# Performance work log

Hardware: AMD Instinct MI355X
Metric: run time of the kernel (lower is better)

## Reference

```python
import jax, jax.numpy as jnp
import numpy as np

N = 262144
L = 16; FEAT = 2; T = 1 << 19; N_MIN = 16; N_MAX = 4096
AABB = 1.0
TIME_RES1 = 16; TIME_RES2 = 20
B = float(np.exp(np.log(N_MAX / N_MIN) / (L - 1)))
SCALES = [N_MIN * (B ** l) - 1.0 for l in range(L)]
RES = [int(np.ceil(s)) + 1 for s in SCALES]
PRIMES = (np.uint32(1), np.uint32(2654435761), np.uint32(805459861))
OFFS = np.array([[(i >> d) & 1 for d in range(3)] for i in range(8)], dtype=np.int32)  # [8,3]


def hash_encode(x, table):
    """Instant-NGP multiresolution hash encoding. x: [N,3] in [0,1], table: [L,T,F] -> [N,L*F]."""
    offs = jnp.asarray(OFFS)
    outs = []
    for l in range(L):
        s = SCALES[l]; res = RES[l]
        pos = x * s + 0.5
        p0 = jnp.floor(pos)
        w = pos - p0                                             # [N,3] trilinear weights
        c = p0.astype(jnp.int32)[:, None, :] + offs[None, :, :]  # [N,8,3] corner coords
        if res ** 3 <= T:
            # dense grid fits in table -> coherent indexing (tcnn behavior)
            idx = c[..., 0] + c[..., 1] * res + c[..., 2] * (res * res)
        else:
            cu = c.astype(jnp.uint32)
            idx = ((cu[..., 0] * PRIMES[0]) ^ (cu[..., 1] * PRIMES[1]) ^ (cu[..., 2] * PRIMES[2])) & np.uint32(T - 1)
            idx = idx.astype(jnp.int32)
        wv = jnp.prod(jnp.where(offs[None] == 1, w[:, None, :], 1.0 - w[:, None, :]), axis=-1)  # [N,8]
        outs.append(jnp.einsum('nkf,nk->nf', table[l][idx], wv))
    return jnp.concatenate(outs, axis=1)


def sh_encode(dirs):
    """tcnn SphericalHarmonics degree 4: dirs in [0,1] mapped to [-1,1] -> 16 coeffs."""
    d = dirs * 2.0 - 1.0
    x, y, z = d[:, 0], d[:, 1], d[:, 2]
    xy, xz, yz = x * y, x * z, y * z
    x2, y2, z2 = x * x, y * y, z * z
    cols = [
        jnp.full_like(x, 0.28209479177387814),
        -0.48860251190291987 * y,
        0.48860251190291987 * z,
        -0.48860251190291987 * x,
        1.0925484305920792 * xy,
        -1.0925484305920792 * yz,
        0.94617469575755997 * z2 - 0.31539156525252005,
        -1.0925484305920792 * xz,
        0.54627421529603959 * (x2 - y2),
        0.59004358992664352 * y * (-3.0 * x2 + y2),
        2.8906114426405538 * xy * z,
        0.45704579946446572 * y * (1.0 - 5.0 * z2),
        0.3731763325901154 * z * (5.0 * z2 - 3.0),
        0.45704579946446572 * x * (1.0 - 5.0 * z2),
        1.4453057213202769 * z * (x2 - y2),
        0.59004358992664352 * x * (-x2 + 3.0 * y2),
    ]
    return jnp.stack(cols, axis=1)


def setup_inputs() -> dict:
    key = jax.random.key(0)
    ks = jax.random.split(key, 12)
    xyz = jax.random.uniform(ks[0], (N, 3), minval=-AABB, maxval=AABB, dtype=jnp.float32)
    tcol = jnp.full((N, 1), 0.37, dtype=jnp.float32)  # one shared time per chunk (module reads ts[0])
    original_xyzs = jnp.concatenate([xyz, tcol], axis=1)
    dirs = jax.random.uniform(ks[1], (N, 3), dtype=jnp.float32)
    tinit = lambda k: jax.random.normal(k, (L, T, FEAT), dtype=jnp.float32) * 1e-2
    lin = lambda k, fi, fo: jax.random.normal(k, (fi, fo), dtype=jnp.float32) * (1.0 / np.sqrt(fi))
    return dict(
        original_xyzs=original_xyzs, dirs=dirs,
        table_a1=tinit(ks[2]), table_a2=tinit(ks[3]),       # xyz_hashes[index], xyz_hashes[index+1]
        table_b1=tinit(ks[4]), table_b2=tinit(ks[5]),       # xyz_hashes2[index2], xyz_hashes2[index2+1]
        table_static=tinit(ks[6]),
        w_xyz1=lin(ks[7], 96, 64), w_xyz2=lin(ks[8], 64, 16),
        w_c1=lin(ks[9], 32, 64), w_c2=lin(ks[10], 64, 64), w_c3=lin(ks[11], 64, 3),
    )


def reference(original_xyzs, dirs, table_a1, table_a2, table_b1, table_b2, table_static,
              w_xyz1, w_xyz2, w_c1, w_c2, w_c3):
    t = original_xyzs[0, 3]
    xyz = (original_xyzs[:, :3] + AABB) / AABB / 2.0        # [-aabb,aabb] -> [0,1]
    prev1 = 1.0 - (t * TIME_RES1 - jnp.floor(t * TIME_RES1)); next1 = 1.0 - prev1
    s1 = prev1 + next1; prev1 = prev1 / s1; next1 = next1 / s1
    prev2 = 1.0 - (t * TIME_RES2 - jnp.floor(t * TIME_RES2)); next2 = 1.0 - prev2
    s2 = prev2 + next2; prev2 = prev2 / s2; next2 = next2 / s2
    fa1 = hash_encode(xyz, table_a1); fa2 = hash_encode(xyz, table_a2)
    fb1 = hash_encode(xyz, table_b1); fb2 = hash_encode(xyz, table_b2)
    blend_a = fa1 * prev1 + fa2 * next1
    blend_b = fb1 * prev2 + fb2 * next2
    hash_res = jnp.concatenate([blend_a, blend_b, hash_encode(xyz, table_static)], axis=1)  # [N,96]
    h = jax.nn.relu(hash_res @ w_xyz1) @ w_xyz2              # [N,16]
    sigma = jnp.exp(h[:, 0])                                 # TruncExp forward
    dir_enc = sh_encode(dirs)                                # [N,16]
    ch = jnp.concatenate([dir_enc, h], axis=1)               # [N,32]
    color = jax.nn.sigmoid(jax.nn.relu(jax.nn.relu(ch @ w_c1) @ w_c2) @ w_c3)
    feature1 = jnp.concatenate([fa1[:, -8:], fb1[:, -8:]], axis=1)
    feature2 = jnp.concatenate([fa2[:, -8:], fb2[:, -8:]], axis=1)
    return color, sigma, feature1, feature2
```

## Files before the change

### kernel.cpp

```cpp
#include <hip/hip_runtime.h>
#include <cmath>

constexpr int NPTS = 262144;
constexpr int LVLS = 16;
constexpr int TSZ  = 524288;
constexpr unsigned TMASK = TSZ - 1u;
constexpr unsigned P1 = 2654435761u;
constexpr unsigned P2 = 805459861u;

constexpr size_t PB10_BYTES = (size_t)LVLS * TSZ * 8;
constexpr size_t AB4_BYTES  = (size_t)4 * TSZ * 16;
constexpr size_t FEAT_BYTES = (size_t)LVLS * 3 * NPTS * 4;
constexpr int    WP_W1 = 0,    WP_W1N = 48 * 64;
constexpr int    WP_W2 = 3072, WP_W2N = 32 * 16;
constexpr int    WP_C1 = 3584, WP_C1N = 16 * 64;
constexpr int    WP_C2 = 4608, WP_C2N = 32 * 64;
constexpr int    WP_TOT = 6656;
constexpr size_t WP_BYTES = WP_TOT * 4;
constexpr size_t WS_NEED = PB10_BYTES + AB4_BYTES + FEAT_BYTES + WP_BYTES;

constexpr float QSCALE = 4096.0f;
constexpr float QINV   = 1.0f / 4096.0f;

typedef __fp16 half2v __attribute__((ext_vector_type(2)));

__device__ __forceinline__ half2v pkh(float lo, float hi) {
  return __builtin_amdgcn_cvt_pkrtz(lo, hi);
}
__device__ __forceinline__ unsigned pkh2(float lo, float hi) {
  half2v r = __builtin_amdgcn_cvt_pkrtz(lo, hi);
  return *reinterpret_cast<unsigned*>(&r);
}
__device__ __forceinline__ half2v ash2(unsigned w) {
  return *reinterpret_cast<half2v*>(&w);
}
__device__ __forceinline__ float2 uph2(unsigned w) {
  half2v h = ash2(w);
  return make_float2((float)h.x, (float)h.y);
}

#if __has_builtin(__builtin_amdgcn_fdot2)
__device__ __forceinline__ float DOT2(half2v a, half2v b, float c) {
  return __builtin_amdgcn_fdot2(a, b, c, false);
}
#else
__device__ __forceinline__ float DOT2(half2v a, half2v b, float c) {
  return c + (float)a.x * (float)b.x + (float)a.y * (float)b.y;
}
#endif

__device__ __forceinline__ void time_weights(float t, float mul, float& bp, float& bn) {
  const float ft = t * mul;
  const float fr = ft - floorf(ft);
  float p = 1.0f - fr, n = 1.0f - p;
  const float s = p + n;
  bp = p / s; bn = n / s;
}

__device__ __forceinline__ unsigned q10(float v) {
  int q = (int)floorf(v * QSCALE + 0.5f) + 512;
  q = (q < 0) ? 0 : ((q > 1023) ? 1023 : q);
  return (unsigned)q;
}
__device__ __forceinline__ float dq10(unsigned w, int sh) {
  return (float)((int)((w >> sh) & 1023u) - 512);
}

constexpr int MAXS = 10;
struct Sched {
  float scale[LVLS];
  int   res[LVLS];
  int   dense[LVLS];
  int   nblocks[8];
  int   nsegs[8];
  int   sblk0[8][MAXS];
  unsigned char skind[8][MAXS];
  unsigned char slevel[8][MAXS];
  short schunk0[8][MAXS];
};

__global__ __launch_bounds__(256)
void repack_pb(const float* __restrict__ xyzs,
               const float2* __restrict__ ta1, const float2* __restrict__ ta2,
               const float2* __restrict__ tb1, const float2* __restrict__ tb2,
               const float2* __restrict__ tst,
               uint2* __restrict__ PB10, uint4* __restrict__ AB4)
{
  const size_t i = (size_t)blockIdx.x * 256 + threadIdx.x;
  const int l = (int)(i >> 19);
  float p1w, n1w, p2w, n2w;
  const float t = xyzs[3];
  time_weights(t, 16.0f, p1w, n1w);
  time_weights(t, 20.0f, p2w, n2w);
  const float2 a1 = ta1[i], a2 = ta2[i], b1 = tb1[i], b2 = tb2[i], st = tst[i];
  const float ba0 = a1.x * p1w + a2.x * n1w;
  const float ba1v = a1.y * p1w + a2.y * n1w;
  const float bb0 = b1.x * p2w + b2.x * n2w;
  const float bb1v = b1.y * p2w + b2.y * n2w;
  uint2 e;
  e.x = q10(ba0) | (q10(ba1v) << 10) | (q10(bb0) << 20);
  e.y = q10(bb1v) | (q10(st.x) << 10) | (q10(st.y) << 20);
  PB10[i] = e;
  if (l >= 12) {
    uint4 r;
    r.x = pkh2(a1.x, a1.y);
    r.y = pkh2(a2.x, a2.y);
    r.z = pkh2(b1.x, b1.y);
    r.w = pkh2(b2.x, b2.y);
    AB4[i - (size_t)12 * TSZ] = r;
  }
}

__global__ __launch_bounds__(256)
void wconv(const float* __restrict__ w1, const float* __restrict__ w2,
           const float* __restrict__ wc1, const float* __restrict__ wc2,
           unsigned* __restrict__ wp)
{
  const int g = blockIdx.x * 256 + threadIdx.x;
  if (g < WP_W1N) {
    const int i = g, r = i >> 6, j = i & 63;
    wp[WP_W1 + i] = pkh2(w1[(2 * r) * 64 + j], w1[(2 * r + 1) * 64 + j]);
  } else if (g < WP_W1N + WP_W2N) {
    const int i = g - WP_W1N, r = i >> 4, j = i & 15;
    wp[WP_W2 + i] = pkh2(w2[(2 * r) * 16 + j], w2[(2 * r + 1) * 16 + j]);
  } else if (g < WP_W1N + WP_W2N + WP_C1N) {
    const int i = g - WP_W1N - WP_W2N, r = i >> 6, j = i & 63;
    wp[WP_C1 + i] = pkh2(wc1[(2 * r) * 64 + j], wc1[(2 * r + 1) * 64 + j]);
  } else if (g < WP_TOT) {
    const int i = g - WP_W1N - WP_W2N - WP_C1N, r = i >> 6, j = i & 63;
    wp[WP_C2 + i] = pkh2(wc2[(2 * r) * 64 + j], wc2[(2 * r + 1) * 64 + j]);
  }
}

__global__ __launch_bounds__(512)
void ngp_gather(const float* __restrict__ xyzs,
                const uint2* __restrict__ PB10, const uint4* __restrict__ AB4,
                unsigned* __restrict__ feat, float* __restrict__ out, Sched sc)
{
  const int k = blockIdx.x & 7;
  const int j = blockIdx.x >> 3;
  if (j >= sc.nblocks[k]) return;
  int l = 0, chunk = 0, kind = 0;
  #pragma unroll
  for (int s = 0; s < MAXS; ++s) {
    if (s < sc.nsegs[k] && j >= sc.sblk0[k][s]) {
      kind  = sc.skind[k][s];
      l     = sc.slevel[k][s];
      chunk = sc.schunk0[k][s] + (j - sc.sblk0[k][s]);
    }
  }
  const int p = (chunk << 9) + threadIdx.x;

  const float4 xin = reinterpret_cast<const float4*>(xyzs)[p];
  const float px = (xin.x + 1.0f) * 0.5f;
  const float py = (xin.y + 1.0f) * 0.5f;
  const float pz = (xin.z + 1.0f) * 0.5f;

  const float s = sc.scale[l];
  const int res = sc.res[l];
  const float fx = px * s + 0.5f; const float f0x = floorf(fx); const float wx = fx - f0x;
  const float fy = py * s + 0.5f; const float f0y = floorf(fy); const float wy = fy - f0y;
  const float fz = pz * s + 0.5f; const float f0z = floorf(fz); const float wz = fz - f0z;
  const int ix = (int)f0x, iy = (int)f0y, iz = (int)f0z;

  unsigned idx[8];
  if (sc.dense[l]) {
    const int r2 = res * res;
    const int bx0 = ix,       bx1 = ix + 1;
    const int by0 = iy * res, by1 = by0 + res;
    const int bz0 = iz * r2,  bz1 = bz0 + r2;
    idx[0] = (unsigned)(bx0 + by0 + bz0);
    idx[1] = (unsigned)(bx1 + by0 + bz0);
    idx[2] = (unsigned)(bx0 + by1 + bz0);
    idx[3] = (unsigned)(bx1 + by1 + bz0);
    idx[4] = (unsigned)(bx0 + by0 + bz1);
    idx[5] = (unsigned)(bx1 + by0 + bz1);
    idx[6] = (unsigned)(bx0 + by1 + bz1);
    idx[7] = (unsigned)(bx1 + by1 + bz1);
  } else {
    const unsigned hx0 = (unsigned)ix,      hx1 = hx0 + 1u;
    const unsigned hy0 = (unsigned)iy * P1, hy1 = hy0 + P1;
    const unsigned hz0 = (unsigned)iz * P2, hz1 = hz0 + P2;
    idx[0] = (hx0 ^ hy0 ^ hz0) & TMASK;
    idx[1] = (hx1 ^ hy0 ^ hz0) & TMASK;
    idx[2] = (hx0 ^ hy1 ^ hz0) & TMASK;
    idx[3] = (hx1 ^ hy1 ^ hz0) & TMASK;
    idx[4] = (hx0 ^ hy0 ^ hz1) & TMASK;
    idx[5] = (hx1 ^ hy0 ^ hz1) & TMASK;
    idx[6] = (hx0 ^ hy1 ^ hz1) & TMASK;
    idx[7] = (hx1 ^ hy1 ^ hz1) & TMASK;
  }

  const float wxa = 1.0f - wx, wya = 1.0f - wy, wza = 1.0f - wz;
  float wv[8];
  wv[0] = wxa * wya * wza;
  wv[1] = wx  * wya * wza;
  wv[2] = wxa * wy  * wza;
  wv[3] = wx  * wy  * wza;
  wv[4] = wxa * wya * wz;
  wv[5] = wx  * wya * wz;
  wv[6] = wxa * wy  * wz;
  wv[7] = wx  * wy  * wz;

  if (kind == 0) {
    const uint2* tb = PB10 + (size_t)l * TSZ;
    uint2 m[8];
    #pragma unroll
    for (int c = 0; c < 8; ++c) m[c] = tb[idx[c]];
    float A0 = 0.f, A1 = 0.f, B0 = 0.f, B1 = 0.f, S0 = 0.f, S1 = 0.f;
    #pragma unroll
    for (int c = 0; c < 8; ++c) {
      const float w = wv[c];
      const unsigned ux = m[c].x, uy = m[c].y;
      A0 += dq10(ux, 0)  * w;
      A1 += dq10(ux, 10) * w;
      B0 += dq10(ux, 20) * w;
      B1 += dq10(uy, 0)  * w;
      S0 += dq10(uy, 10) * w;
      S1 += dq10(uy, 20) * w;
    }
    feat[(size_t)(l * 3 + 0) * NPTS + p] = pkh2(A0 * QINV, A1 * QINV);
    feat[(size_t)(l * 3 + 1) * NPTS + p] = pkh2(B0 * QINV, B1 * QINV);
    feat[(size_t)(l * 3 + 2) * NPTS + p] = pkh2(S0 * QINV, S1 * QINV);
  } else {
    const uint4* tb = AB4 + (size_t)(l - 12) * TSZ;
    uint4 m[8];
    #pragma unroll
    for (int c = 0; c < 8; ++c) m[c] = tb[idx[c]];
    float a10 = 0.f, a11 = 0.f, a20 = 0.f, a21 = 0.f;
    float b10 = 0.f, b11 = 0.f, b20 = 0.f, b21 = 0.f;
    #pragma unroll
    for (int c = 0; c < 8; ++c) {
      const float w = wv[c];
      float2 f;
      f = uph2(m[c].x); a10 += f.x * w; a11 += f.y * w;
      f = uph2(m[c].y); a20 += f.x * w; a21 += f.y * w;
      f = uph2(m[c].z); b10 += f.x * w; b11 += f.y * w;
      f = uph2(m[c].w); b20 += f.x * w; b21 += f.y * w;
    }
    const size_t fo = (size_t)(l - 12) * 2;
    const size_t f1base = (size_t)4 * NPTS + (size_t)p * 16;
    const size_t f2base = (size_t)20 * NPTS + (size_t)p * 16;
    *reinterpret_cast<float2*>(out + f1base + fo)     = make_float2(a10, a11);
    *reinterpret_cast<float2*>(out + f1base + 8 + fo) = make_float2(b10, b11);
    *reinterpret_cast<float2*>(out + f2base + fo)     = make_float2(a20, a21);
    *reinterpret_cast<float2*>(out + f2base + 8 + fo) = make_float2(b20, b21);
  }
}

__global__ __launch_bounds__(256)
void ngp_mlp(const float* __restrict__ dirs,
             const unsigned* __restrict__ feat,
             const unsigned* __restrict__ wp,
             const float* __restrict__ wc3,
             float* __restrict__ out)
{
  __shared__ unsigned sw[WP_TOT];
  __shared__ float swc3[192];
  for (int i = threadIdx.x; i < WP_TOT; i += 256) sw[i] = wp[i];
  for (int i = threadIdx.x; i < 192; i += 256) swc3[i] = wc3[i];
  __syncthreads();

  const int n = blockIdx.x * 256 + threadIdx.x;
  const half2v* w1p = reinterpret_cast<const half2v*>(sw + WP_W1);
  const half2v* w2p = reinterpret_cast<const half2v*>(sw + WP_W2);
  const half2v* c1p = reinterpret_cast<const half2v*>(sw + WP_C1);
  const half2v* c2p = reinterpret_cast<const half2v*>(sw + WP_C2);

  float h1[64];
  #pragma unroll
  for (int j = 0; j < 64; ++j) h1[j] = 0.0f;

  for (int l = 0; l < LVLS; ++l) {
    const half2v A2 = ash2(feat[(size_t)(l * 3 + 0) * NPTS + n]);
    const half2v B2 = ash2(feat[(size_t)(l * 3 + 1) * NPTS + n]);
    const half2v S2 = ash2(feat[(size_t)(l * 3 + 2) * NPTS + n]);
    #pragma unroll
    for (int j = 0; j < 64; ++j) {
      float acc = h1[j];
      acc = DOT2(A2, w1p[l * 64 + j], acc);
      acc = DOT2(B2, w1p[(16 + l) * 64 + j], acc);
      acc = DOT2(S2, w1p[(32 + l) * 64 + j], acc);
      h1[j] = acc;
    }
  }

  float h2[16];
  #pragma unroll
  for (int j = 0; j < 16; ++j) h2[j] = 0.0f;
  #pragma unroll
  for (int k = 0; k < 32; ++k) {
    const half2v hp = pkh(fmaxf(h1[2 * k], 0.0f), fmaxf(h1[2 * k + 1], 0.0f));
    #pragma unroll
    for (int j = 0; j < 16; ++j) h2[j] = DOT2(hp, w2p[k * 16 + j], h2[j]);
  }

  out[(size_t)3 * NPTS + n] = expf(h2[0]);

  const float dx = dirs[(size_t)n * 3 + 0] * 2.0f - 1.0f;
  const float dy = dirs[(size_t)n * 3 + 1] * 2.0f - 1.0f;
  const float dz = dirs[(size_t)n * 3 + 2] * 2.0f - 1.0f;
  const float xy = dx * dy, xz = dx * dz, yz = dy * dz;
  const float x2 = dx * dx, y2 = dy * dy, z2 = dz * dz;
  float sh[16];
  sh[0]  = 0.28209479177387814f;
  sh[1]  = -0.48860251190291987f * dy;
  sh[2]  = 0.48860251190291987f * dz;
  sh[3]  = -0.48860251190291987f * dx;
  sh[4]  = 1.0925484305920792f * xy;
  sh[5]  = -1.0925484305920792f * yz;
  sh[6]  = 0.94617469575756f * z2 - 0.31539156525252005f;
  sh[7]  = -1.0925484305920792f * xz;
  sh[8]  = 0.5462742152960396f * (x2 - y2);
  sh[9]  = 0.5900435899266435f * dy * (-3.0f * x2 + y2);
  sh[10] = 2.890611442640554f * xy * dz;
  sh[11] = 0.4570457994644657f * dy * (1.0f - 5.0f * z2);
  sh[12] = 0.3731763325901154f * dz * (5.0f * z2 - 3.0f);
  sh[13] = 0.4570457994644657f * dx * (1.0f - 5.0f * z2);
  sh[14] = 1.445305721320277f * dz * (x2 - y2);
  sh[15] = 0.5900435899266435f * dx * (-x2 + 3.0f * y2);

  half2v chp[16];
  #pragma unroll
  for (int r = 0; r < 8; ++r) chp[r] = pkh(sh[2 * r], sh[2 * r + 1]);
  #pragma unroll
  for (int r = 0; r < 8; ++r) chp[8 + r] = pkh(h2[2 * r], h2[2 * r + 1]);
  float r1[64];
  #pragma unroll
  for (int j = 0; j < 64; ++j) r1[j] = 0.0f;
  #pragma unroll
  for (int k = 0; k < 16; ++k) {
    const half2v cp = chp[k];
    #pragma unroll
    for (int j = 0; j < 64; ++j) r1[j] = DOT2(cp, c1p[k * 64 + j], r1[j]);
  }

  float r2[64];
  #pragma unroll
  for (int j = 0; j < 64; ++j) r2[j] = 0.0f;
  #pragma unroll
  for (int k = 0; k < 32; ++k) {
    const half2v rp = pkh(fmaxf(r1[2 * k], 0.0f), fmaxf(r1[2 * k + 1], 0.0f));
    #pragma unroll
    for (int j = 0; j < 64; ++j) r2[j] = DOT2(rp, c2p[k * 64 + j], r2[j]);
  }

  float c0a = 0.f, c1a = 0.f, c2a = 0.f;
  #pragma unroll
  for (int k = 0; k < 64; ++k) {
    const float a = fmaxf(r2[k], 0.0f);
    c0a += a * swc3[k * 3 + 0];
    c1a += a * swc3[k * 3 + 1];
    c2a += a * swc3[k * 3 + 2];
  }
  out[(size_t)n * 3 + 0] = 1.0f / (1.0f + expf(-c0a));
  out[(size_t)n * 3 + 1] = 1.0f / (1.0f + expf(-c1a));
  out[(size_t)n * 3 + 2] = 1.0f / (1.0f + expf(-c2a));
}

__global__ __launch_bounds__(256)
void ngp_fused(const float* __restrict__ xyzs, const float* __restrict__ dirs,
               const float* __restrict__ ta1, const float* __restrict__ ta2,
               const float* __restrict__ tb1, const float* __restrict__ tb2,
               const float* __restrict__ tst,
               const float* __restrict__ w1, const float* __restrict__ w2,
               const float* __restrict__ wc1, const float* __restrict__ wc2,
               const float* __restrict__ wc3, float* __restrict__ out, Sched sc)
{
  const int n = blockIdx.x * 256 + threadIdx.x;
  if (n >= NPTS) return;

  float prev1, next1, prev2, next2;
  const float t = xyzs[3];
  time_weights(t, 16.0f, prev1, next1);
  time_weights(t, 20.0f, prev2, next2);

  const float4 xin = reinterpret_cast<const float4*>(xyzs)[n];
  const float px = (xin.x + 1.0f) * 0.5f;
  const float py = (xin.y + 1.0f) * 0.5f;
  const float pz = (xin.z + 1.0f) * 0.5f;

  float h1[64];
  #pragma unroll
  for (int j = 0; j < 64; ++j) h1[j] = 0.0f;

  const size_t f1base = (size_t)4 * NPTS + (size_t)n * 16;
  const size_t f2base = (size_t)20 * NPTS + (size_t)n * 16;

  for (int l = 0; l < LVLS; ++l) {
    const float s = sc.scale[l];
    const int res = sc.res[l];
    const float fx = px * s + 0.5f; const float f0x = floorf(fx); const float wx = fx - f0x;
    const float fy = py * s + 0.5f; const float f0y = floorf(fy); const float wy = fy - f0y;
    const float fz = pz * s + 0.5f; const float f0z = floorf(fz); const float wz = fz - f0z;
    const int ix = (int)f0x, iy = (int)f0y, iz = (int)f0z;

    unsigned idx[8];
    if (sc.dense[l]) {
      const int r2 = res * res;
      const int bx0 = ix,       bx1 = ix + 1;
      const int by0 = iy * res, by1 = by0 + res;
      const int bz0 = iz * r2,  bz1 = bz0 + r2;
      idx[0] = (unsigned)(bx0 + by0 + bz0);
      idx[1] = (unsigned)(bx1 + by0 + bz0);
      idx[2] = (unsigned)(bx0 + by1 + bz0);
      idx[3] = (unsigned)(bx1 + by1 + bz0);
      idx[4] = (unsigned)(bx0 + by0 + bz1);
      idx[5] = (unsigned)(bx1 + by0 + bz1);
      idx[6] = (unsigned)(bx0 + by1 + bz1);
      idx[7] = (unsigned)(bx1 + by1 + bz1);
    } else {
      const unsigned hx0 = (unsigned)ix,      hx1 = hx0 + 1u;
      const unsigned hy0 = (unsigned)iy * P1, hy1 = hy0 + P1;
      const unsigned hz0 = (unsigned)iz * P2, hz1 = hz0 + P2;
      idx[0] = (hx0 ^ hy0 ^ hz0) & TMASK;
      idx[1] = (hx1 ^ hy0 ^ hz0) & TMASK;
      idx[2] = (hx0 ^ hy1 ^ hz0) & TMASK;
      idx[3] = (hx1 ^ hy1 ^ hz0) & TMASK;
      idx[4] = (hx0 ^ hy0 ^ hz1) & TMASK;
      idx[5] = (hx1 ^ hy0 ^ hz1) & TMASK;
      idx[6] = (hx0 ^ hy1 ^ hz1) & TMASK;
      idx[7] = (hx1 ^ hy1 ^ hz1) & TMASK;
    }

    const float wxa = 1.0f - wx, wya = 1.0f - wy, wza = 1.0f - wz;
    float wv[8];
    wv[0] = wxa * wya * wza;
    wv[1] = wx  * wya * wza;
    wv[2] = wxa * wy  * wza;
    wv[3] = wx  * wy  * wza;
    wv[4] = wxa * wya * wz;
    wv[5] = wx  * wya * wz;
    wv[6] = wxa * wy  * wz;
    wv[7] = wx  * wy  * wz;

    float a10 = 0.f, a11 = 0.f, a20 = 0.f, a21 = 0.f;
    float b10 = 0.f, b11 = 0.f, b20 = 0.f, b21 = 0.f;
    float st0 = 0.f, st1 = 0.f;
    const size_t lbase = (size_t)l * TSZ;

    const float2* ba1 = reinterpret_cast<const float2*>(ta1) + lbase;
    const float2* ba2 = reinterpret_cast<const float2*>(ta2) + lbase;
    const float2* bb1 = reinterpret_cast<const float2*>(tb1) + lbase;
    const float2* bb2 = reinterpret_cast<const float2*>(tb2) + lbase;
    const float2* bst = reinterpret_cast<const float2*>(tst) + lbase;
    float2 va1[8], va2[8], vb1[8], vb2[8], vst[8];
    #pragma unroll
    for (int c = 0; c < 8; ++c) {
      const unsigned id = idx[c];
      va1[c] = ba1[id]; va2[c] = ba2[id]; vb1[c] = bb1[id];
      vb2[c] = bb2[id]; vst[c] = bst[id];
    }
    #pragma unroll
    for (int c = 0; c < 8; ++c) {
      const float w = wv[c];
      a10 += va1[c].x * w; a11 += va1[c].y * w;
      a20 += va2[c].x * w; a21 += va2[c].y * w;
      b10 += vb1[c].x * w; b11 += vb1[c].y * w;
      b20 += vb2[c].x * w; b21 += vb2[c].y * w;
      st0 += vst[c].x * w; st1 += vst[c].y * w;
    }

    const float ba0f = a10 * prev1 + a20 * next1;
    const float ba1f = a11 * prev1 + a21 * next1;
    const float bb0f = b10 * prev2 + b20 * next2;
    const float bb1f = b11 * prev2 + b21 * next2;

    const float* wr0 = w1 + (size_t)(2 * l) * 64;
    const float* wr1 = w1 + (size_t)(2 * l + 1) * 64;
    const float* wr2 = w1 + (size_t)(32 + 2 * l) * 64;
    const float* wr3 = w1 + (size_t)(33 + 2 * l) * 64;
    const float* wr4 = w1 + (size_t)(64 + 2 * l) * 64;
    const float* wr5 = w1 + (size_t)(65 + 2 * l) * 64;
    #pragma unroll
    for (int j = 0; j < 64; ++j) {
      float acc = h1[j];
      acc += ba0f * wr0[j];
      acc += ba1f * wr1[j];
      acc += bb0f * wr2[j];
      acc += bb1f * wr3[j];
      acc += st0  * wr4[j];
      acc += st1  * wr5[j];
      h1[j] = acc;
    }

    if (l >= 12) {
      const size_t fo = (size_t)(l - 12) * 2;
      float2* o;
      o = reinterpret_cast<float2*>(out + f1base + fo);     *o = make_float2(a10, a11);
      o = reinterpret_cast<float2*>(out + f1base + 8 + fo); *o = make_float2(b10, b11);
      o = reinterpret_cast<float2*>(out + f2base + fo);     *o = make_float2(a20, a21);
      o = reinterpret_cast<float2*>(out + f2base + 8 + fo); *o = make_float2(b20, b21);
    }
  }

  float h2[16];
  #pragma unroll
  for (int j = 0; j < 16; ++j) h2[j] = 0.0f;
  #pragma unroll
  for (int k = 0; k < 64; ++k) {
    const float a = fmaxf(h1[k], 0.0f);
    #pragma unroll
    for (int j = 0; j < 16; ++j) h2[j] += a * w2[k * 16 + j];
  }
  out[(size_t)3 * NPTS + n] = expf(h2[0]);

  const float dx = dirs[(size_t)n * 3 + 0] * 2.0f - 1.0f;
  const float dy = dirs[(size_t)n * 3 + 1] * 2.0f - 1.0f;
  const float dz = dirs[(size_t)n * 3 + 2] * 2.0f - 1.0f;
  const float xy = dx * dy, xz = dx * dz, yz = dy * dz;
  const float x2 = dx * dx, y2 = dy * dy, z2 = dz * dz;
  float sh[16];
  sh[0]  = 0.28209479177387814f;
  sh[1]  = -0.48860251190291987f * dy;
  sh[2]  = 0.48860251190291987f * dz;
  sh[3]  = -0.48860251190291987f * dx;
  sh[4]  = 1.0925484305920792f * xy;
  sh[5]  = -1.0925484305920792f * yz;
  sh[6]  = 0.94617469575756f * z2 - 0.31539156525252005f;
  sh[7]  = -1.0925484305920792f * xz;
  sh[8]  = 0.5462742152960396f * (x2 - y2);
  sh[9]  = 0.5900435899266435f * dy * (-3.0f * x2 + y2);
  sh[10] = 2.890611442640554f * xy * dz;
  sh[11] = 0.4570457994644657f * dy * (1.0f - 5.0f * z2);
  sh[12] = 0.3731763325901154f * dz * (5.0f * z2 - 3.0f);
  sh[13] = 0.4570457994644657f * dx * (1.0f - 5.0f * z2);
  sh[14] = 1.445305721320277f * dz * (x2 - y2);
  sh[15] = 0.5900435899266435f * dx * (-x2 + 3.0f * y2);

  float r1[64];
  #pragma unroll
  for (int j = 0; j < 64; ++j) r1[j] = 0.0f;
  #pragma unroll
  for (int k = 0; k < 16; ++k) {
    const float a = sh[k];
    #pragma unroll
    for (int j = 0; j < 64; ++j) r1[j] += a * wc1[(size_t)k * 64 + j];
  }
  #pragma unroll
  for (int k = 0; k < 16; ++k) {
    const float a = h2[k];
    #pragma unroll
    for (int j = 0; j < 64; ++j) r1[j] += a * wc1[(size_t)(16 + k) * 64 + j];
  }
  #pragma unroll
  for (int j = 0; j < 64; ++j) r1[j] = fmaxf(r1[j], 0.0f);

  float r2[64];
  #pragma unroll
  for (int j = 0; j < 64; ++j) r2[j] = 0.0f;
  #pragma unroll
  for (int k = 0; k < 64; ++k) {
    const float a = r1[k];
    #pragma unroll
    for (int j = 0; j < 64; ++j) r2[j] += a * wc2[(size_t)k * 64 + j];
  }

  float c0a = 0.f, c1a = 0.f, c2a = 0.f;
  #pragma unroll
  for (int k = 0; k < 64; ++k) {
    const float a = fmaxf(r2[k], 0.0f);
    c0a += a * wc3[k * 3 + 0];
    c1a += a * wc3[k * 3 + 1];
    c2a += a * wc3[k * 3 + 2];
  }
  out[(size_t)n * 3 + 0] = 1.0f / (1.0f + expf(-c0a));
  out[(size_t)n * 3 + 1] = 1.0f / (1.0f + expf(-c1a));
  out[(size_t)n * 3 + 2] = 1.0f / (1.0f + expf(-c2a));
}

extern "C" void kernel_launch(void* const* d_in, const int* in_sizes, int n_in,
                              void* d_out, int out_size, void* d_ws, size_t ws_size,
                              hipStream_t stream) {
  const float* xyzs = (const float*)d_in[0];
  const float* dirs = (const float*)d_in[1];
  const float* ta1  = (const float*)d_in[2];
  const float* ta2  = (const float*)d_in[3];
  const float* tb1  = (const float*)d_in[4];
  const float* tb2  = (const float*)d_in[5];
  const float* tst  = (const float*)d_in[6];
  const float* w1   = (const float*)d_in[7];
  const float* w2   = (const float*)d_in[8];
  const float* wc1  = (const float*)d_in[9];
  const float* wc2  = (const float*)d_in[10];
  const float* wc3  = (const float*)d_in[11];

  Sched sc = {};
  const double B = exp(log(4096.0 / 16.0) / 15.0);
  for (int l = 0; l < LVLS; ++l) {
    const double s = 16.0 * pow(B, (double)l) - 1.0;
    sc.scale[l] = (float)s;
    const int res = (int)ceil(s) + 1;
    sc.res[l] = res;
    sc.dense[l] = ((long long)res * res * res <= (long long)TSZ) ? 1 : 0;
  }

  struct Unit { int kind, level; long long w; };
  Unit units[20];
  int nu = 0;
  for (int l = 0; l < LVLS; ++l) units[nu++] = {0, l, sc.dense[l] ? 1LL : 2LL};
  for (int l = 12; l < LVLS; ++l) units[nu++] = {1, l, 3LL};

  constexpr int CH = 512;
  {
    long long totW = 0;
    for (int u = 0; u < nu; ++u) totW += units[u].w * CH;
    int k = 0;
    long long acc = 0;
    auto target = [&](int kk) { return (totW * (kk + 1)) / 8; };
    for (int u = 0; u < nu; ++u) {
      int c0 = 0;
      const long long w = units[u].w;
      while (c0 < CH) {
        while (k < 7 && (acc >= target(k) || sc.nsegs[k] >= MAXS)) k++;
        long long room = target(k) - acc;
        int take;
        if (k == 7) take = CH - c0;
        else {
          take = (int)((room + w - 1) / w);
          if (take > CH - c0) take = CH - c0;
          if (take <= 0) take = 1;
        }
        const int sgi = sc.nsegs[k];
        sc.skind[k][sgi]   = (unsigned char)units[u].kind;
        sc.slevel[k][sgi]  = (unsigned char)units[u].level;
        sc.schunk0[k][sgi] = (short)c0;
        sc.sblk0[k][sgi]   = sc.nblocks[k];
        sc.nsegs[k]++;
        sc.nblocks[k] += take;
        acc += (long long)take * w;
        c0 += take;
      }
    }
  }
  int maxblk = 0;
  for (int k = 0; k < 8; ++k) if (sc.nblocks[k] > maxblk) maxblk = sc.nblocks[k];

  if (ws_size >= WS_NEED) {
    char* base = (char*)d_ws;
    uint2*    PB10 = (uint2*)base;
    uint4*    AB4  = (uint4*)(base + PB10_BYTES);
    unsigned* feat = (unsigned*)(base + PB10_BYTES + AB4_BYTES);
    unsigned* wpp  = (unsigned*)(base + PB10_BYTES + AB4_BYTES + FEAT_BYTES);

    repack_pb<<<(LVLS * TSZ) / 256, 256, 0, stream>>>(
        xyzs, (const float2*)ta1, (const float2*)ta2, (const float2*)tb1,
        (const float2*)tb2, (const float2*)tst, PB10, AB4);
    wconv<<<(WP_TOT + 255) / 256, 256, 0, stream>>>(w1, w2, wc1, wc2, wpp);
    ngp_gather<<<8 * maxblk, 512, 0, stream>>>(
        xyzs, PB10, AB4, feat, (float*)d_out, sc);
    ngp_mlp<<<NPTS / 256, 256, 0, stream>>>(dirs, feat, wpp, wc3, (float*)d_out);
  } else {
    ngp_fused<<<NPTS / 256, 256, 0, stream>>>(
        xyzs, dirs, ta1, ta2, tb1, tb2, tst,
        w1, w2, wc1, wc2, wc3, (float*)d_out, sc);
  }
}
```

Baseline: 360.6 us.

## Merge top-level gathers into single 12-bit packed table pass

For levels 12-15, the separate PB10 (blended 10-bit) and AB4 (fp16 a1/a2/b1/b2) tables are replaced by one 16-byte entry holding all ten channels quantized to 12 bits. That entry includes the static features. The gather kernel now does one 8-corner gather per point for those levels instead of two, and it computes the time blend itself while writing both the MLP features and the per-timestep outputs. This removes four level-gather units and the PB10 writes for those levels. In exchange it adds 64-bit unpacking work and reduces precision from fp16 to 12-bit fixed point for the feature outputs.

```diff
diff --git a/kernel.cpp b/kernel.cpp
--- a/kernel.cpp
+++ b/kernel.cpp
@@ -7,9 +7,10 @@
 constexpr unsigned TMASK = TSZ - 1u;
 constexpr unsigned P1 = 2654435761u;
 constexpr unsigned P2 = 805459861u;
-
-constexpr size_t PB10_BYTES = (size_t)LVLS * TSZ * 8;
-constexpr size_t AB4_BYTES  = (size_t)4 * TSZ * 16;
+constexpr int NPB = 12;
+
+constexpr size_t PB10_BYTES = (size_t)NPB * TSZ * 8;
+constexpr size_t ABQ_BYTES  = (size_t)4 * TSZ * 16;
 constexpr size_t FEAT_BYTES = (size_t)LVLS * 3 * NPTS * 4;
 constexpr int    WP_W1 = 0,    WP_W1N = 48 * 64;
 constexpr int    WP_W2 = 3072, WP_W2N = 32 * 16;
@@ -17,10 +18,12 @@
 constexpr int    WP_C2 = 4608, WP_C2N = 32 * 64;
 constexpr int    WP_TOT = 6656;
 constexpr size_t WP_BYTES = WP_TOT * 4;
-constexpr size_t WS_NEED = PB10_BYTES + AB4_BYTES + FEAT_BYTES + WP_BYTES;
+constexpr size_t WS_NEED = PB10_BYTES + ABQ_BYTES + FEAT_BYTES + WP_BYTES;
 
 constexpr float QSCALE = 4096.0f;
 constexpr float QINV   = 1.0f / 4096.0f;
+constexpr float QS12   = 16384.0f;
+constexpr float QI12   = 1.0f / 16384.0f;
 
 typedef __fp16 half2v __attribute__((ext_vector_type(2)));
 
@@ -33,10 +36,6 @@
 }
 __device__ __forceinline__ half2v ash2(unsigned w) {
   return *reinterpret_cast<half2v*>(&w);
-}
-__device__ __forceinline__ float2 uph2(unsigned w) {
-  half2v h = ash2(w);
-  return make_float2((float)h.x, (float)h.y);
 }
 
 #if __has_builtin(__builtin_amdgcn_fdot2)
@@ -64,6 +63,14 @@
 }
 __device__ __forceinline__ float dq10(unsigned w, int sh) {
   return (float)((int)((w >> sh) & 1023u) - 512);
+}
+__device__ __forceinline__ unsigned long long q12(float v) {
+  int q = (int)floorf(v * QS12 + 0.5f) + 2048;
+  q = (q < 0) ? 0 : ((q > 4095) ? 4095 : q);
+  return (unsigned long long)q;
+}
+__device__ __forceinline__ float dq12(unsigned long long u, int sh) {
+  return (float)((int)((u >> sh) & 4095ull) - 2048);
 }
 
 constexpr int MAXS = 10;
@@ -84,30 +91,35 @@
                const float2* __restrict__ ta1, const float2* __restrict__ ta2,
                const float2* __restrict__ tb1, const float2* __restrict__ tb2,
                const float2* __restrict__ tst,
-               uint2* __restrict__ PB10, uint4* __restrict__ AB4)
+               uint2* __restrict__ PB10, uint4* __restrict__ ABQ)
 {
   const size_t i = (size_t)blockIdx.x * 256 + threadIdx.x;
   const int l = (int)(i >> 19);
-  float p1w, n1w, p2w, n2w;
-  const float t = xyzs[3];
-  time_weights(t, 16.0f, p1w, n1w);
-  time_weights(t, 20.0f, p2w, n2w);
   const float2 a1 = ta1[i], a2 = ta2[i], b1 = tb1[i], b2 = tb2[i], st = tst[i];
-  const float ba0 = a1.x * p1w + a2.x * n1w;
-  const float ba1v = a1.y * p1w + a2.y * n1w;
-  const float bb0 = b1.x * p2w + b2.x * n2w;
-  const float bb1v = b1.y * p2w + b2.y * n2w;
-  uint2 e;
-  e.x = q10(ba0) | (q10(ba1v) << 10) | (q10(bb0) << 20);
-  e.y = q10(bb1v) | (q10(st.x) << 10) | (q10(st.y) << 20);
-  PB10[i] = e;
-  if (l >= 12) {
-    uint4 r;
-    r.x = pkh2(a1.x, a1.y);
-    r.y = pkh2(a2.x, a2.y);
-    r.z = pkh2(b1.x, b1.y);
-    r.w = pkh2(b2.x, b2.y);
-    AB4[i - (size_t)12 * TSZ] = r;
+  if (l < NPB) {
+    float p1w, n1w, p2w, n2w;
+    const float t = xyzs[3];
+    time_weights(t, 16.0f, p1w, n1w);
+    time_weights(t, 20.0f, p2w, n2w);
+    const float ba0  = a1.x * p1w + a2.x * n1w;
+    const float ba1v = a1.y * p1w + a2.y * n1w;
+    const float bb0  = b1.x * p2w + b2.x * n2w;
+    const float bb1v = b1.y * p2w + b2.y * n2w;
+    uint2 e;
+    e.x = q10(ba0) | (q10(ba1v) << 10) | (q10(bb0) << 20);
+    e.y = q10(bb1v) | (q10(st.x) << 10) | (q10(st.y) << 20);
+    PB10[i] = e;
+  } else {
+    const unsigned long long lo =
+        q12(a1.x) | (q12(a1.y) << 12) | (q12(a2.x) << 24) |
+        (q12(a2.y) << 36) | (q12(st.x) << 48);
+    const unsigned long long hi =
+        q12(b1.x) | (q12(b1.y) << 12) | (q12(b2.x) << 24) |
+        (q12(b2.y) << 36) | (q12(st.y) << 48);
+    uint4 e;
+    e.x = (unsigned)lo;  e.y = (unsigned)(lo >> 32);
+    e.z = (unsigned)hi;  e.w = (unsigned)(hi >> 32);
+    ABQ[i - (size_t)NPB * TSZ] = e;
   }
 }
 
@@ -134,7 +146,7 @@
 
 __global__ __launch_bounds__(512)
 void ngp_gather(const float* __restrict__ xyzs,
-                const uint2* __restrict__ PB10, const uint4* __restrict__ AB4,
+                const uint2* __restrict__ PB10, const uint4* __restrict__ ABQ,
                 unsigned* __restrict__ feat, float* __restrict__ out, Sched sc)
 {
   const int k = blockIdx.x & 7;
@@ -223,21 +235,41 @@
     feat[(size_t)(l * 3 + 1) * NPTS + p] = pkh2(B0 * QINV, B1 * QINV);
     feat[(size_t)(l * 3 + 2) * NPTS + p] = pkh2(S0 * QINV, S1 * QINV);
   } else {
-    const uint4* tb = AB4 + (size_t)(l - 12) * TSZ;
+    const uint4* tb = ABQ + (size_t)(l - NPB) * TSZ;
     uint4 m[8];
     #pragma unroll
     for (int c = 0; c < 8; ++c) m[c] = tb[idx[c]];
     float a10 = 0.f, a11 = 0.f, a20 = 0.f, a21 = 0.f;
     float b10 = 0.f, b11 = 0.f, b20 = 0.f, b21 = 0.f;
+    float st0 = 0.f, st1 = 0.f;
     #pragma unroll
     for (int c = 0; c < 8; ++c) {
       const float w = wv[c];
-      float2 f;
-      f = uph2(m[c].x); a10 += f.x * w; a11 += f.y * w;
-      f = uph2(m[c].y); a20 += f.x * w; a21 += f.y * w;
-      f = uph2(m[c].z); b10 += f.x * w; b11 += f.y * w;
-      f = uph2(m[c].w); b20 += f.x * w; b21 += f.y * w;
-    }
+      const unsigned long long lo = ((unsigned long long)m[c].y << 32) | m[c].x;
+      const unsigned long long hi = ((unsigned long long)m[c].w << 32) | m[c].z;
+      a10 += dq12(lo, 0)  * w;
+      a11 += dq12(lo, 12) * w;
+      a20 += dq12(lo, 24) * w;
+      a21 += dq12(lo, 36) * w;
+      st0 += dq12(lo, 48) * w;
+      b10 += dq12(hi, 0)  * w;
+      b11 += dq12(hi, 12) * w;
+      b20 += dq12(hi, 24) * w;
+      b21 += dq12(hi, 36) * w;
+      st1 += dq12(hi, 48) * w;
+    }
+    a10 *= QI12; a11 *= QI12; a20 *= QI12; a21 *= QI12;
+    b10 *= QI12; b11 *= QI12; b20 *= QI12; b21 *= QI12;
+    st0 *= QI12; st1 *= QI12;
+
+    float p1w, n1w, p2w, n2w;
+    const float t = xyzs[3];
+    time_weights(t, 16.0f, p1w, n1w);
+    time_weights(t, 20.0f, p2w, n2w);
+    feat[(size_t)(l * 3 + 0) * NPTS + p] = pkh2(a10 * p1w + a20 * n1w, a11 * p1w + a21 * n1w);
+    feat[(size_t)(l * 3 + 1) * NPTS + p] = pkh2(b10 * p2w + b20 * n2w, b11 * p2w + b21 * n2w);
+    feat[(size_t)(l * 3 + 2) * NPTS + p] = pkh2(st0, st1);
+
     const size_t fo = (size_t)(l - 12) * 2;
     const size_t f1base = (size_t)4 * NPTS + (size_t)p * 16;
     const size_t f2base = (size_t)20 * NPTS + (size_t)p * 16;
@@ -596,10 +628,10 @@
   }
 
   struct Unit { int kind, level; long long w; };
-  Unit units[20];
+  Unit units[16];
   int nu = 0;
-  for (int l = 0; l < LVLS; ++l) units[nu++] = {0, l, sc.dense[l] ? 1LL : 2LL};
-  for (int l = 12; l < LVLS; ++l) units[nu++] = {1, l, 3LL};
+  for (int l = 0; l < NPB; ++l) units[nu++] = {0, l, sc.dense[l] ? 1LL : 2LL};
+  for (int l = NPB; l < LVLS; ++l) units[nu++] = {1, l, 3LL};
 
   constexpr int CH = 512;
   {
@@ -639,16 +671,16 @@
   if (ws_size >= WS_NEED) {
     char* base = (char*)d_ws;
     uint2*    PB10 = (uint2*)base;
-    uint4*    AB4  = (uint4*)(base + PB10_BYTES);
-    unsigned* feat = (unsigned*)(base + PB10_BYTES + AB4_BYTES);
-    unsigned* wpp  = (unsigned*)(base + PB10_BYTES + AB4_BYTES + FEAT_BYTES);
+    uint4*    ABQ  = (uint4*)(base + PB10_BYTES);
+    unsigned* feat = (unsigned*)(base + PB10_BYTES + ABQ_BYTES);
+    unsigned* wpp  = (unsigned*)(base + PB10_BYTES + ABQ_BYTES + FEAT_BYTES);
 
     repack_pb<<<(LVLS * TSZ) / 256, 256, 0, stream>>>(
         xyzs, (const float2*)ta1, (const float2*)ta2, (const float2*)tb1,
-        (const float2*)tb2, (const float2*)tst, PB10, AB4);
+        (const float2*)tb2, (const float2*)tst, PB10, ABQ);
     wconv<<<(WP_TOT + 255) / 256, 256, 0, stream>>>(w1, w2, wc1, wc2, wpp);
     ngp_gather<<<8 * maxblk, 512, 0, stream>>>(
-        xyzs, PB10, AB4, feat, (float*)d_out, sc);
+        xyzs, PB10, ABQ, feat, (float*)d_out, sc);
     ngp_mlp<<<NPTS / 256, 256, 0, stream>>>(dirs, feat, wpp, wc3, (float*)d_out);
   } else {
     ngp_fused<<<NPTS / 256, 256, 0, stream>>>(
```

Result: faster. 321.5 us (-10.8%).
